# Kernel optimization log

Measured on AMD Instinct MI355X. Metric: run time of the kernel, lower is better.

Reference implementation:

```python
import jax, jax.numpy as jnp
import numpy as np

N_NODES = 50000
N_RAND_EDGES = 800000
LEAKY_SLOPE = 0.2


def gat_layer(x, edge_index, W, a_src, a_dst, b, num_heads):
    """Multi-head GAT layer. W: [Din, Dout]; heads split Dout; concat output."""
    N = x.shape[0]
    Dout = W.shape[1]
    Dh = Dout // num_heads
    z = (x @ W).reshape(N, num_heads, Dh)                      # [N,H,Dh]
    src = edge_index[0]
    dst = edge_index[1]
    alpha_src = jnp.einsum('nhd,hd->nh', z, a_src)             # [N,H]
    alpha_dst = jnp.einsum('nhd,hd->nh', z, a_dst)             # [N,H]
    e = jax.nn.leaky_relu(alpha_src[src] + alpha_dst[dst], LEAKY_SLOPE)  # [E,H]
    # segment softmax over incoming edges of each dst node
    m = jax.ops.segment_max(e, dst, num_segments=N)            # [N,H]
    e = jnp.exp(e - m[dst])
    denom = jax.ops.segment_sum(e, dst, num_segments=N)        # [N,H]
    alpha = e / (denom[dst] + 1e-16)                           # [E,H]
    msg = z[src] * alpha[:, :, None]                           # [E,H,Dh]
    out = jax.ops.segment_sum(msg, dst, num_segments=N)        # [N,H,Dh]
    return out.reshape(N, Dout) + b


def setup_inputs() -> dict:
    key = jax.random.key(0)
    ks = jax.random.split(key, 12)
    input_dim, hidden_dim, num_classes, num_heads = 128, 64, 16, 8
    x = jax.random.normal(ks[0], (N_NODES, input_dim), dtype=jnp.float32)
    rand_edges = jax.random.randint(ks[1], (2, N_RAND_EDGES), 0, N_NODES, dtype=jnp.int32)
    self_loops = jnp.tile(jnp.arange(N_NODES, dtype=jnp.int32), (2, 1))
    edge_indices = jnp.concatenate([rand_edges, self_loops], axis=1)   # [2, 850000]

    def glorot(k, shape):
        fan = sum(shape[-2:]) if len(shape) > 1 else shape[0]
        return jax.random.normal(k, shape, dtype=jnp.float32) * (2.0 / fan) ** 0.5

    W1 = glorot(ks[2], (input_dim, hidden_dim))
    a_src1 = glorot(ks[3], (num_heads, hidden_dim // num_heads))
    a_dst1 = glorot(ks[4], (num_heads, hidden_dim // num_heads))
    b1 = jnp.zeros((hidden_dim,), dtype=jnp.float32)
    W2 = glorot(ks[5], (hidden_dim, num_classes))
    a_src2 = glorot(ks[6], (1, num_classes))
    a_dst2 = glorot(ks[7], (1, num_classes))
    b2 = jnp.zeros((num_classes,), dtype=jnp.float32)
    return {"x": x, "edge_indices": edge_indices,
            "W1": W1, "a_src1": a_src1, "a_dst1": a_dst1, "b1": b1,
            "W2": W2, "a_src2": a_src2, "a_dst2": a_dst2, "b2": b2}


def reference(x, edge_indices, W1, a_src1, a_dst1, b1, W2, a_src2, a_dst2, b2):
    # Dropout is identity in eval mode.
    h = gat_layer(x, edge_indices, W1, a_src1, a_dst1, b1, num_heads=8)
    h = jax.nn.elu(h)
    return gat_layer(h, edge_indices, W2, a_src2, a_dst2, b2, num_heads=1)
```

## Files before the change

kernel.cpp:

```cpp
#include <hip/hip_runtime.h>
#include <hip/hip_fp16.h>


#define LRELU(v) ((v) > 0.f ? (v) : 0.2f * (v))

__global__ void kA(const float* __restrict__ x, const float* __restrict__ W1,
                   const float* __restrict__ a_src1, const float* __restrict__ a_dst1,
                   const int* __restrict__ src, const int* __restrict__ dst,
                   int* __restrict__ deg, unsigned short* __restrict__ csr,
                   __half* __restrict__ z1h, float* __restrict__ as1,
                   float* __restrict__ ad1, int N, int E) {
    __shared__ float xs[64][132];
    __shared__ float wt[64][132];
    __shared__ float avs[128];
    int b = blockIdx.x;
    int tid = threadIdx.x;
    bool is_gemm = (b < 1564) && ((b & 1) == 0);

    if (!is_gemm) {
        int rank = (b < 1564) ? (b >> 1) : (b - 782);
        for (int e = rank * 256 + tid; e < E; e += 1024 * 256) {
            int d = dst[e];
            int pos = atomicAdd(&deg[d], 1);
            if (pos < 64) csr[(d << 6) + pos] = (unsigned short)src[e];
        }
        return;
    }

    int n0 = (b >> 1) * 64;
    for (int idx = tid; idx < 8192; idx += 256) {
        int k = idx >> 6, c = idx & 63;
        wt[c][k] = W1[idx];
    }
    for (int idx = tid; idx < 2048; idx += 256) {
        int r = idx >> 5, q = idx & 31;
        int n = n0 + r; if (n >= N) n = N - 1;
        float4 v = ((const float4*)(x + (size_t)n * 128))[q];
        *(float4*)&xs[r][q * 4] = v;
    }
    if (tid < 128) avs[tid] = (tid < 64) ? a_src1[tid] : a_dst1[tid - 64];
    __syncthreads();

    int rg = tid >> 4, cg2 = tid & 15;
    float acc[4][4] = {};
    for (int k4 = 0; k4 < 32; ++k4) {
        float4 xv[4], wv[4];
#pragma unroll
        for (int i = 0; i < 4; ++i) xv[i] = *(const float4*)&xs[rg * 4 + i][k4 * 4];
#pragma unroll
        for (int j = 0; j < 4; ++j) wv[j] = *(const float4*)&wt[cg2 * 4 + j][k4 * 4];
#pragma unroll
        for (int i = 0; i < 4; ++i)
#pragma unroll
            for (int j = 0; j < 4; ++j) {
                acc[i][j] += xv[i].x * wv[j].x;
                acc[i][j] += xv[i].y * wv[j].y;
                acc[i][j] += xv[i].z * wv[j].z;
                acc[i][j] += xv[i].w * wv[j].w;
            }
    }
    int h = cg2 >> 1, db = (cg2 & 1) * 4;
    float pas[4], pad_[4];
#pragma unroll
    for (int i = 0; i < 4; ++i) {
        float s = 0.f, dd = 0.f;
#pragma unroll
        for (int j = 0; j < 4; ++j) {
            s  += acc[i][j] * avs[h * 8 + db + j];
            dd += acc[i][j] * avs[64 + h * 8 + db + j];
        }
        pas[i] = s; pad_[i] = dd;
    }
#pragma unroll
    for (int i = 0; i < 4; ++i) {
        pas[i]  += __shfl_xor(pas[i], 1, 64);
        pad_[i] += __shfl_xor(pad_[i], 1, 64);
    }
#pragma unroll
    for (int i = 0; i < 4; ++i) {
        int n = n0 + rg * 4 + i;
        if (n < N) {
            union { __half2 h2[2]; uint2 u; } pk;
            pk.h2[0] = __floats2half2_rn(acc[i][0], acc[i][1]);
            pk.h2[1] = __floats2half2_rn(acc[i][2], acc[i][3]);
            *(uint2*)&z1h[(size_t)n * 64 + cg2 * 4] = pk.u;
            if ((cg2 & 1) == 0) {
                as1[(size_t)n * 8 + h] = pas[i];
                ad1[(size_t)n * 8 + h] = pad_[i];
            }
        }
    }
}

__global__ void kg1(const int* __restrict__ deg, const unsigned short* __restrict__ csr,
                    const float* __restrict__ as1, const float* __restrict__ ad1,
                    const __half* __restrict__ z1h, const float* __restrict__ b1,
                    const float* __restrict__ W2, const float* __restrict__ a_src2,
                    const float* __restrict__ a_dst2,
                    float* __restrict__ z2, float* __restrict__ as2,
                    float* __restrict__ ad2, int N) {
    __shared__ int s_idx[4][64];
    __shared__ float asv[4][64][8];
    __shared__ float hs[4][64];
    int lane = threadIdx.x & 63, wid = threadIdx.x >> 6;
    int d = blockIdx.x * 4 + wid;
    if (d >= N) return;
    int q = lane & 7, g = lane >> 3;
    int cnt = min(deg[d], 64);
    float adv = ad1[(size_t)d * 8 + q];
    if (lane < cnt) {
        int s = csr[(d << 6) + lane];
        s_idx[wid][lane] = s;
        const float4* ap = (const float4*)(as1 + (size_t)s * 8);
        float4 u = ap[0], v = ap[1];
        *(float4*)&asv[wid][lane][0] = u;
        *(float4*)&asv[wid][lane][4] = v;
    }
    float a0 = 0.f, a1 = 0.f, a2 = 0.f, a3 = 0.f;
    float a4 = 0.f, a5 = 0.f, a6 = 0.f, a7 = 0.f, dsum = 0.f;
#pragma unroll 2
    for (int j = g; j < cnt; j += 8) {
        int s = s_idx[wid][j];
        float ev = asv[wid][j][q] + adv;
        float w = __expf(LRELU(ev));
        float4 raw = *(const float4*)(z1h + (size_t)s * 64 + q * 8);
        const __half2* hp = (const __half2*)&raw;
        float2 f0 = __half22float2(hp[0]), f1 = __half22float2(hp[1]);
        float2 f2 = __half22float2(hp[2]), f3 = __half22float2(hp[3]);
        a0 += w * f0.x; a1 += w * f0.y; a2 += w * f1.x; a3 += w * f1.y;
        a4 += w * f2.x; a5 += w * f2.y; a6 += w * f3.x; a7 += w * f3.y;
        dsum += w;
    }
#pragma unroll
    for (int m = 8; m <= 32; m <<= 1) {
        a0 += __shfl_xor(a0, m, 64); a1 += __shfl_xor(a1, m, 64);
        a2 += __shfl_xor(a2, m, 64); a3 += __shfl_xor(a3, m, 64);
        a4 += __shfl_xor(a4, m, 64); a5 += __shfl_xor(a5, m, 64);
        a6 += __shfl_xor(a6, m, 64); a7 += __shfl_xor(a7, m, 64);
        dsum += __shfl_xor(dsum, m, 64);
    }
    float inv = 1.f / dsum;
    float hv[8] = {a0 * inv + b1[q * 8 + 0], a1 * inv + b1[q * 8 + 1],
                   a2 * inv + b1[q * 8 + 2], a3 * inv + b1[q * 8 + 3],
                   a4 * inv + b1[q * 8 + 4], a5 * inv + b1[q * 8 + 5],
                   a6 * inv + b1[q * 8 + 6], a7 * inv + b1[q * 8 + 7]};
#pragma unroll
    for (int i = 0; i < 8; ++i) hv[i] = hv[i] > 0.f ? hv[i] : expm1f(hv[i]);
    if (g == 0) {
        *(float4*)&hs[wid][q * 8]     = make_float4(hv[0], hv[1], hv[2], hv[3]);
        *(float4*)&hs[wid][q * 8 + 4] = make_float4(hv[4], hv[5], hv[6], hv[7]);
    }
    int kq = lane >> 4, c = lane & 15;
    float zc = 0.f;
#pragma unroll
    for (int k = 0; k < 16; ++k)
        zc += hs[wid][kq * 16 + k] * W2[(kq * 16 + k) * 16 + c];
    zc += __shfl_xor(zc, 16, 64);
    zc += __shfl_xor(zc, 32, 64);
    float ps = zc * a_src2[c];
    float pd = zc * a_dst2[c];
#pragma unroll
    for (int m = 1; m < 16; m <<= 1) {
        ps += __shfl_xor(ps, m, 64);
        pd += __shfl_xor(pd, m, 64);
    }
    if (lane < 16) z2[(size_t)d * 16 + lane] = zc;
    if (lane == 0) { as2[d] = ps; ad2[d] = pd; }
}

__global__ void kg2(const int* __restrict__ deg, const unsigned short* __restrict__ csr,
                    const float* __restrict__ as2, const float* __restrict__ ad2,
                    const float* __restrict__ z2, const float* __restrict__ b2,
                    float* __restrict__ out, int N) {
    __shared__ int s_idx[4][64];
    __shared__ float asv[4][64];
    int lane = threadIdx.x & 63, wid = threadIdx.x >> 6;
    int d = blockIdx.x * 4 + wid;
    if (d >= N) return;
    int q = lane & 3, g = lane >> 2;
    int cnt = min(deg[d], 64);
    float adv = ad2[d];
    if (lane < cnt) {
        int s = csr[(d << 6) + lane];
        s_idx[wid][lane] = s;
        asv[wid][lane] = as2[s];
    }
    float ax = 0.f, ay = 0.f, az = 0.f, aw = 0.f, dsum = 0.f;
#pragma unroll 2
    for (int j = g; j < cnt; j += 16) {
        int s = s_idx[wid][j];
        float ev = asv[wid][j] + adv;
        float w = __expf(LRELU(ev));
        float4 zv = *(const float4*)(z2 + (size_t)s * 16 + q * 4);
        ax += w * zv.x; ay += w * zv.y; az += w * zv.z; aw += w * zv.w;
        dsum += w;
    }
#pragma unroll
    for (int m = 4; m <= 32; m <<= 1) {
        ax += __shfl_xor(ax, m, 64); ay += __shfl_xor(ay, m, 64);
        az += __shfl_xor(az, m, 64); aw += __shfl_xor(aw, m, 64);
        dsum += __shfl_xor(dsum, m, 64);
    }
    if (g == 0) {
        float inv = 1.f / dsum;
        float4 o = make_float4(ax * inv + b2[q * 4], ay * inv + b2[q * 4 + 1],
                               az * inv + b2[q * 4 + 2], aw * inv + b2[q * 4 + 3]);
        *(float4*)&out[(size_t)d * 16 + q * 4] = o;
    }
}

extern "C" void kernel_launch(void* const* d_in, const int* in_sizes, int n_in,
                              void* d_out, int out_size, void* d_ws, size_t ws_size,
                              hipStream_t stream) {
    const float* x      = (const float*)d_in[0];
    const int*   ei     = (const int*)d_in[1];
    const float* W1     = (const float*)d_in[2];
    const float* a_src1 = (const float*)d_in[3];
    const float* a_dst1 = (const float*)d_in[4];
    const float* b1     = (const float*)d_in[5];
    const float* W2     = (const float*)d_in[6];
    const float* a_src2 = (const float*)d_in[7];
    const float* a_dst2 = (const float*)d_in[8];
    const float* b2     = (const float*)d_in[9];
    float* out = (float*)d_out;

    const int N = in_sizes[0] / 128;
    const int E = in_sizes[1] / 2;
    const int* src = ei;
    const int* dst = ei + E;

    float* ws = (float*)d_ws;
    size_t off = 0;
    __half* z1h = (__half*)(ws + off); off += (size_t)N * 32;
    float* as1 = ws + off; off += (size_t)N * 8;
    float* ad1 = ws + off; off += (size_t)N * 8;
    float* z2  = ws + off; off += (size_t)N * 16;
    float* as2 = ws + off; off += (size_t)N;
    float* ad2 = ws + off; off += (size_t)N;
    unsigned short* csr = (unsigned short*)(ws + off); off += (size_t)N * 32;
    int* deg = (int*)(ws + off); off += (size_t)N;

    hipMemsetAsync(deg, 0, (size_t)N * sizeof(int), stream);

    kA<<<1806, 256, 0, stream>>>(x, W1, a_src1, a_dst1, src, dst, deg, csr,
                                 z1h, as1, ad1, N, E);
    kg1<<<(N + 3) / 4, 256, 0, stream>>>(deg, csr, as1, ad1, z1h, b1, W2,
                                         a_src2, a_dst2, z2, as2, ad2, N);
    kg2<<<(N + 3) / 4, 256, 0, stream>>>(deg, csr, as2, ad2, z2, b2, out, N);
}
```

Before: 189.4 us.

## Interleave degree counters with CSR slots and store layer-2 features in fp16

Replaces the separate degree array and CSR slot array with one padded per-node bucket that holds the atomic counter next to the source slots. The atomic increment and slot write then hit the same cache region, and the later readers fetch count and neighbours together. Layer-2 projected features are also stored as half precision to halve the gather traffic in the final aggregation. In exchange the whole bucket array must be zeroed each call, which is a much larger memset, and z2 loses precision.

```diff
diff --git a/kernel.cpp b/kernel.cpp
--- a/kernel.cpp
+++ b/kernel.cpp
@@ -3,11 +3,12 @@
 
 
 #define LRELU(v) ((v) > 0.f ? (v) : 0.2f * (v))
+#define BKT_STRIDE 192
 
 __global__ void kA(const float* __restrict__ x, const float* __restrict__ W1,
                    const float* __restrict__ a_src1, const float* __restrict__ a_dst1,
                    const int* __restrict__ src, const int* __restrict__ dst,
-                   int* __restrict__ deg, unsigned short* __restrict__ csr,
+                   char* __restrict__ bkt,
                    __half* __restrict__ z1h, float* __restrict__ as1,
                    float* __restrict__ ad1, int N, int E) {
     __shared__ float xs[64][132];
@@ -21,8 +22,10 @@
         int rank = (b < 1564) ? (b >> 1) : (b - 782);
         for (int e = rank * 256 + tid; e < E; e += 1024 * 256) {
             int d = dst[e];
-            int pos = atomicAdd(&deg[d], 1);
-            if (pos < 64) csr[(d << 6) + pos] = (unsigned short)src[e];
+            int* cnt = (int*)(bkt + (size_t)d * BKT_STRIDE);
+            int pos = atomicAdd(cnt, 1);
+            if (pos < 64)
+                ((unsigned short*)(cnt + 1))[pos] = (unsigned short)src[e];
         }
         return;
     }
@@ -92,12 +95,12 @@
     }
 }
 
-__global__ void kg1(const int* __restrict__ deg, const unsigned short* __restrict__ csr,
+__global__ void kg1(const char* __restrict__ bkt,
                     const float* __restrict__ as1, const float* __restrict__ ad1,
                     const __half* __restrict__ z1h, const float* __restrict__ b1,
                     const float* __restrict__ W2, const float* __restrict__ a_src2,
                     const float* __restrict__ a_dst2,
-                    float* __restrict__ z2, float* __restrict__ as2,
+                    __half* __restrict__ z2h, float* __restrict__ as2,
                     float* __restrict__ ad2, int N) {
     __shared__ int s_idx[4][64];
     __shared__ float asv[4][64][8];
@@ -106,10 +109,12 @@
     int d = blockIdx.x * 4 + wid;
     if (d >= N) return;
     int q = lane & 7, g = lane >> 3;
-    int cnt = min(deg[d], 64);
+    const char* bp = bkt + (size_t)d * BKT_STRIDE;
+    int cnt = min(*(const int*)bp, 64);
+    const unsigned short* slots = (const unsigned short*)(bp + 4);
     float adv = ad1[(size_t)d * 8 + q];
     if (lane < cnt) {
-        int s = csr[(d << 6) + lane];
+        int s = slots[lane];
         s_idx[wid][lane] = s;
         const float4* ap = (const float4*)(as1 + (size_t)s * 8);
         float4 u = ap[0], v = ap[1];
@@ -164,13 +169,13 @@
         ps += __shfl_xor(ps, m, 64);
         pd += __shfl_xor(pd, m, 64);
     }
-    if (lane < 16) z2[(size_t)d * 16 + lane] = zc;
+    if (lane < 16) z2h[(size_t)d * 16 + lane] = __float2half_rn(zc);
     if (lane == 0) { as2[d] = ps; ad2[d] = pd; }
 }
 
-__global__ void kg2(const int* __restrict__ deg, const unsigned short* __restrict__ csr,
+__global__ void kg2(const char* __restrict__ bkt,
                     const float* __restrict__ as2, const float* __restrict__ ad2,
-                    const float* __restrict__ z2, const float* __restrict__ b2,
+                    const __half* __restrict__ z2h, const float* __restrict__ b2,
                     float* __restrict__ out, int N) {
     __shared__ int s_idx[4][64];
     __shared__ float asv[4][64];
@@ -178,10 +183,12 @@
     int d = blockIdx.x * 4 + wid;
     if (d >= N) return;
     int q = lane & 3, g = lane >> 2;
-    int cnt = min(deg[d], 64);
+    const char* bp = bkt + (size_t)d * BKT_STRIDE;
+    int cnt = min(*(const int*)bp, 64);
+    const unsigned short* slots = (const unsigned short*)(bp + 4);
     float adv = ad2[d];
     if (lane < cnt) {
-        int s = csr[(d << 6) + lane];
+        int s = slots[lane];
         s_idx[wid][lane] = s;
         asv[wid][lane] = as2[s];
     }
@@ -191,8 +198,10 @@
         int s = s_idx[wid][j];
         float ev = asv[wid][j] + adv;
         float w = __expf(LRELU(ev));
-        float4 zv = *(const float4*)(z2 + (size_t)s * 16 + q * 4);
-        ax += w * zv.x; ay += w * zv.y; az += w * zv.z; aw += w * zv.w;
+        uint2 raw = *(const uint2*)(z2h + (size_t)s * 16 + q * 4);
+        const __half2* hp = (const __half2*)&raw;
+        float2 f0 = __half22float2(hp[0]), f1 = __half22float2(hp[1]);
+        ax += w * f0.x; ay += w * f0.y; az += w * f1.x; aw += w * f1.y;
         dsum += w;
     }
 #pragma unroll
@@ -234,17 +243,16 @@
     __half* z1h = (__half*)(ws + off); off += (size_t)N * 32;
     float* as1 = ws + off; off += (size_t)N * 8;
     float* ad1 = ws + off; off += (size_t)N * 8;
-    float* z2  = ws + off; off += (size_t)N * 16;
+    __half* z2h = (__half*)(ws + off); off += (size_t)N * 8;
     float* as2 = ws + off; off += (size_t)N;
     float* ad2 = ws + off; off += (size_t)N;
-    unsigned short* csr = (unsigned short*)(ws + off); off += (size_t)N * 32;
-    int* deg = (int*)(ws + off); off += (size_t)N;
-
-    hipMemsetAsync(deg, 0, (size_t)N * sizeof(int), stream);
-
-    kA<<<1806, 256, 0, stream>>>(x, W1, a_src1, a_dst1, src, dst, deg, csr,
+    char* bkt = (char*)(ws + off); off += (size_t)N * 48;
+
+    hipMemsetAsync(bkt, 0, (size_t)N * BKT_STRIDE, stream);
+
+    kA<<<1806, 256, 0, stream>>>(x, W1, a_src1, a_dst1, src, dst, bkt,
                                  z1h, as1, ad1, N, E);
-    kg1<<<(N + 3) / 4, 256, 0, stream>>>(deg, csr, as1, ad1, z1h, b1, W2,
-                                         a_src2, a_dst2, z2, as2, ad2, N);
-    kg2<<<(N + 3) / 4, 256, 0, stream>>>(deg, csr, as2, ad2, z2, b2, out, N);
-}
+    kg1<<<(N + 3) / 4, 256, 0, stream>>>(bkt, as1, ad1, z1h, b1, W2,
+                                         a_src2, a_dst2, z2h, as2, ad2, N);
+    kg2<<<(N + 3) / 4, 256, 0, stream>>>(bkt, as2, ad2, z2h, b2, out, N);
+}
```

Result: slower. 221.5 us (+17.0%).
